# Kernel tuning notes

Hardware: AMD Instinct MI355X
Metric: run time of the kernel (lower is better)

## Reference

```python
import jax, jax.numpy as jnp
import numpy as np

LOG_N = 12
N = 1 << LOG_N          # 4096, in_size == out_size == n (power of 2, no padding)
NSTACKS = 1
NBLOCKS = 1
BATCH = 8192
INCREASING_STRIDE = True


def setup_inputs() -> dict:
    key = jax.random.key(0)
    k1, k2 = jax.random.split(key)
    x = jax.random.normal(k1, (BATCH, N), dtype=jnp.float32)
    # init='randn': twiddle entries ~ N(0,1) scaled by 1/sqrt(2)
    twiddle = jax.random.normal(k2, (NSTACKS, NBLOCKS, LOG_N, N // 2, 2, 2),
                                dtype=jnp.float32) * (1.0 / np.sqrt(2.0))
    return {"x": x, "twiddle": twiddle}


def _butterfly_multiply(twiddle, inp, increasing_stride):
    # twiddle: (S, nblocks, log_n, n//2, 2, 2); inp: (B, S, n)
    B, S, n = inp.shape
    nblocks, log_n = twiddle.shape[1], twiddle.shape[2]
    out = inp
    cur = increasing_stride
    for blk in range(nblocks):
        for idx in range(log_n):
            log_stride = idx if cur else log_n - 1 - idx
            stride = 1 << log_stride
            d = n // (2 * stride)  # number of diagonal blocks
            # t: (s, d, j, i, k) with j the within-block stride index
            t = twiddle[:, blk, idx].reshape(S, d, stride, 2, 2)
            xr = out.reshape(B, S, d, 2, stride)  # (b, s, d, k, j)
            out = jnp.einsum('sdjik,bsdkj->bsdij', t, xr).reshape(B, S, n)
        cur = not cur
    return out


def reference(x, twiddle):
    B = x.shape[0]
    # pre_process: in_size == n so no padding; nstacks == 1
    inp = x.reshape(B, NSTACKS, N)
    out = _butterfly_multiply(twiddle, inp, INCREASING_STRIDE)
    # post_process: out_size == nstacks * n, bias is None
    return out.reshape(B, NSTACKS * N)
```

## Files before the change

### kernel.cpp

```cpp
#include <hip/hip_runtime.h>
#include <stdint.h>

#define LOG_N 12
#define N 4096
#define NPAIR 2048
#define ROWS 4
#define NT 512

__device__ __forceinline__ int swz(int e){
  return e ^ (((e>>6)&7)<<3) ^ (((e>>3)&1)<<2);
}

template<int LS0>
__device__ __forceinline__ void phase3(float (&v)[ROWS][8], int base,
                                       const float4* __restrict__ twq4){
#pragma unroll
  for(int sub=0; sub<3; ++sub){
    const int ls = LS0 + sub;
    const float4* __restrict__ twq = twq4 + ls*NPAIR;
#pragma unroll
    for(int m=0;m<4;++m){
      const int k0 = (sub==0) ? (2*m) : (sub==1) ? (((m>>1)<<2)|(m&1)) : m;
      const int k1 = k0 + (1<<sub);
      const int pos0 = base + (k0<<LS0);
      const int p = ((pos0>>(ls+1))<<ls) | (pos0 & ((1<<ls)-1));
      const float4 q = twq[p];
#pragma unroll
      for(int r=0;r<ROWS;++r){
        const float x0=v[r][k0], x1=v[r][k1];
        v[r][k0] = fmaf(q.x,x0,q.y*x1);
        v[r][k1] = fmaf(q.z,x0,q.w*x1);
      }
    }
  }
}

__global__ __launch_bounds__(NT, 4)
void butterfly_k(const float* __restrict__ x, const float* __restrict__ tw,
                 float* __restrict__ out)
{
  __shared__ float lds[ROWS*N];
  const int t = threadIdx.x;
  const size_t row0 = (size_t)blockIdx.x * ROWS;
  const float4* twq4 = (const float4*)tw;

  float v[ROWS][8];

  {
    const float4* px = (const float4*)x;
#pragma unroll
    for(int r=0;r<ROWS;++r){
      const float4 a = px[(row0+r)*(N/4) + 2*t];
      const float4 b = px[(row0+r)*(N/4) + 2*t + 1];
      v[r][0]=a.x; v[r][1]=a.y; v[r][2]=a.z; v[r][3]=a.w;
      v[r][4]=b.x; v[r][5]=b.y; v[r][6]=b.z; v[r][7]=b.w;
    }
  }

  phase3<0>(v, 8*t, twq4);

  {
    const int B = (8*t) ^ (((t>>3)&7)<<3);
    const int flip = (t&1)<<2;
#pragma unroll
    for(int r=0;r<ROWS;++r){
      float* L = lds + r*N;
      *(float4*)(L + B + flip)     = make_float4(v[r][0],v[r][1],v[r][2],v[r][3]);
      *(float4*)(L + B + (4^flip)) = make_float4(v[r][4],v[r][5],v[r][6],v[r][7]);
    }
  }
  __syncthreads();
  const int baseB = ((t>>3)<<6) | (t&7);
#pragma unroll
  for(int k=0;k<8;++k){
    const int a = swz(baseB + (k<<3));
#pragma unroll
    for(int r=0;r<ROWS;++r) v[r][k] = lds[r*N + a];
  }

  phase3<3>(v, baseB, twq4);

#pragma unroll
  for(int k=0;k<8;++k){
    const int a = swz(baseB + (k<<3));
#pragma unroll
    for(int r=0;r<ROWS;++r) lds[r*N + a] = v[r][k];
  }
  __syncthreads();
  const int baseC = ((t>>6)<<9) | (t&63);
#pragma unroll
  for(int k=0;k<8;++k){
    const int a = swz(baseC + (k<<6));
#pragma unroll
    for(int r=0;r<ROWS;++r) v[r][k] = lds[r*N + a];
  }

  phase3<6>(v, baseC, twq4);

#pragma unroll
  for(int k=0;k<8;++k){
    const int a = swz(baseC + (k<<6));
#pragma unroll
    for(int r=0;r<ROWS;++r) lds[r*N + a] = v[r][k];
  }
  __syncthreads();
#pragma unroll
  for(int k=0;k<8;++k){
    const int a = swz(t + (k<<9));
#pragma unroll
    for(int r=0;r<ROWS;++r) v[r][k] = lds[r*N + a];
  }

  phase3<9>(v, t, twq4);

#pragma unroll
  for(int r=0;r<ROWS;++r){
    float* po = out + (row0+r)*N + t;
#pragma unroll
    for(int k=0;k<8;++k) po[(size_t)(k<<9)] = v[r][k];
  }
}

extern "C" void kernel_launch(void* const* d_in, const int* in_sizes, int n_in,
                              void* d_out, int out_size, void* d_ws, size_t ws_size,
                              hipStream_t stream) {
  const float* x  = (const float*)d_in[0];
  const float* tw = (const float*)d_in[1];
  float* out = (float*)d_out;
  const int batch = in_sizes[0] / N;
  dim3 grid(batch / ROWS), block(NT);
  hipLaunchKernelGGL(butterfly_k, grid, block, 0, stream, x, tw, out);
}
```

Before: 252.6 us.

## Halve LDS footprint and replace block barriers with wave-local fences

Shrinks the shared buffer from four rows to two and processes the rows in two passes. The first two exchanges stay within a wave (64-element groups owned by 8 or 64 threads), so block-wide __syncthreads are replaced by an LDS waitcnt plus a scheduling barrier. The cross-wave exchange before the last stage keeps full barriers but now runs in two halves. The goal is to cut barrier stalls and LDS usage so more blocks fit per CU, with launch bounds raised to match. The risk is extra serialization, more LDS round trips and register pressure under the tighter launch bound.

```diff
diff --git a/kernel.cpp b/kernel.cpp
--- a/kernel.cpp
+++ b/kernel.cpp
@@ -9,6 +9,11 @@
 
 __device__ __forceinline__ int swz(int e){
   return e ^ (((e>>6)&7)<<3) ^ (((e>>3)&1)<<2);
+}
+
+__device__ __forceinline__ void wave_fence(){
+  asm volatile("s_waitcnt lgkmcnt(0)" ::: "memory");
+  __builtin_amdgcn_sched_barrier(0);
 }
 
 template<int LS0>
@@ -35,11 +40,11 @@
   }
 }
 
-__global__ __launch_bounds__(NT, 4)
+__global__ __launch_bounds__(NT, 8)
 void butterfly_k(const float* __restrict__ x, const float* __restrict__ tw,
                  float* __restrict__ out)
 {
-  __shared__ float lds[ROWS*N];
+  __shared__ float lds[2*N];
   const int t = threadIdx.x;
   const size_t row0 = (size_t)blockIdx.x * ROWS;
   const float4* twq4 = (const float4*)tw;
@@ -59,56 +64,80 @@
 
   phase3<0>(v, 8*t, twq4);
 
+  const int baseB = ((t>>3)<<6) | (t&7);
   {
-    const int B = (8*t) ^ (((t>>3)&7)<<3);
+    const int Bb = (8*t) ^ (((t>>3)&7)<<3);
     const int flip = (t&1)<<2;
 #pragma unroll
-    for(int r=0;r<ROWS;++r){
-      float* L = lds + r*N;
-      *(float4*)(L + B + flip)     = make_float4(v[r][0],v[r][1],v[r][2],v[r][3]);
-      *(float4*)(L + B + (4^flip)) = make_float4(v[r][4],v[r][5],v[r][6],v[r][7]);
+    for(int pp=0;pp<2;++pp){
+      wave_fence();
+#pragma unroll
+      for(int rr=0;rr<2;++rr){
+        float* L = lds + rr*N;
+        const int r = 2*pp + rr;
+        *(float4*)(L + Bb + flip)     = make_float4(v[r][0],v[r][1],v[r][2],v[r][3]);
+        *(float4*)(L + Bb + (4^flip)) = make_float4(v[r][4],v[r][5],v[r][6],v[r][7]);
+      }
+      wave_fence();
+#pragma unroll
+      for(int k=0;k<8;++k){
+        const int a = swz(baseB + (k<<3));
+#pragma unroll
+        for(int rr=0;rr<2;++rr) v[2*pp+rr][k] = lds[rr*N + a];
+      }
     }
-  }
-  __syncthreads();
-  const int baseB = ((t>>3)<<6) | (t&7);
-#pragma unroll
-  for(int k=0;k<8;++k){
-    const int a = swz(baseB + (k<<3));
-#pragma unroll
-    for(int r=0;r<ROWS;++r) v[r][k] = lds[r*N + a];
   }
 
   phase3<3>(v, baseB, twq4);
 
+  const int baseC = ((t>>6)<<9) | (t&63);
 #pragma unroll
-  for(int k=0;k<8;++k){
-    const int a = swz(baseB + (k<<3));
+  for(int pp=0;pp<2;++pp){
+    wave_fence();
 #pragma unroll
-    for(int r=0;r<ROWS;++r) lds[r*N + a] = v[r][k];
+    for(int k=0;k<8;++k){
+      const int a = swz(baseB + (k<<3));
+#pragma unroll
+      for(int rr=0;rr<2;++rr) lds[rr*N + a] = v[2*pp+rr][k];
+    }
+    wave_fence();
+#pragma unroll
+    for(int k=0;k<8;++k){
+      const int a = swz(baseC + (k<<6));
+#pragma unroll
+      for(int rr=0;rr<2;++rr) v[2*pp+rr][k] = lds[rr*N + a];
+    }
   }
-  __syncthreads();
-  const int baseC = ((t>>6)<<9) | (t&63);
+
+  phase3<6>(v, baseC, twq4);
+
+  wave_fence();
 #pragma unroll
   for(int k=0;k<8;++k){
     const int a = swz(baseC + (k<<6));
 #pragma unroll
-    for(int r=0;r<ROWS;++r) v[r][k] = lds[r*N + a];
-  }
-
-  phase3<6>(v, baseC, twq4);
-
-#pragma unroll
-  for(int k=0;k<8;++k){
-    const int a = swz(baseC + (k<<6));
-#pragma unroll
-    for(int r=0;r<ROWS;++r) lds[r*N + a] = v[r][k];
+    for(int rr=0;rr<2;++rr) lds[rr*N + a] = v[rr][k];
   }
   __syncthreads();
 #pragma unroll
   for(int k=0;k<8;++k){
     const int a = swz(t + (k<<9));
 #pragma unroll
-    for(int r=0;r<ROWS;++r) v[r][k] = lds[r*N + a];
+    for(int rr=0;rr<2;++rr) v[rr][k] = lds[rr*N + a];
+  }
+  __syncthreads();
+#pragma unroll
+  for(int k=0;k<8;++k){
+    const int a = swz(baseC + (k<<6));
+#pragma unroll
+    for(int rr=0;rr<2;++rr) lds[rr*N + a] = v[2+rr][k];
+  }
+  __syncthreads();
+#pragma unroll
+  for(int k=0;k<8;++k){
+    const int a = swz(t + (k<<9));
+#pragma unroll
+    for(int rr=0;rr<2;++rr) v[2+rr][k] = lds[rr*N + a];
   }
 
   phase3<9>(v, t, twq4);
```

Result: slower. 400.7 us (+58.6%).
